# Kernel tuning notes

Measured on AMD Instinct MI355X. Metric: run time of the kernel, lower is better.

The kernel has to match this reference:

```python
import jax, jax.numpy as jnp
import numpy as np

B, S, H, E = 64, 1024, 256, 256

def setup_inputs() -> dict:
    key = jax.random.key(0)
    k = jax.random.split(key, 6)
    scale = 1.0 / np.sqrt(H)
    return {
        "data_alpha": jax.random.normal(k[0], (B, S, H), jnp.float32),
        "data_beta": jax.random.normal(k[1], (B, S, H), jnp.float32),
        "data_embed": jax.random.normal(k[2], (B, S, E), jnp.float32),
        "data_mask": jnp.ones((B, S), jnp.float32),
        "Wb": jax.random.normal(k[3], (E, H), jnp.float32) * scale,
        "bb": jnp.zeros((E,), jnp.float32),
        "Wa": jax.random.normal(k[4], (H,), jnp.float32) * scale,
        "ba": jnp.zeros((1,), jnp.float32),
    }

def reference(data_alpha, data_beta, data_embed, data_mask, Wb, bb, Wa, ba):
    # beta gates: tanh(Linear(H->E))  [B,S,E]
    beta_w = jnp.tanh(jnp.einsum('bsh,eh->bse', data_beta, Wb) + bb)
    # alpha logits: Linear(H->1)  [B,S]
    corr = jnp.einsum('bsh,h->bs', data_alpha, Wa) + ba
    attn = jnp.exp(corr)[:, None, :]                       # [B,1,S]
    seq = data_alpha.shape[1]
    flag = jnp.triu(jnp.ones((seq, seq), data_alpha.dtype))[None]  # j >= i
    ef = flag * data_mask[:, None, :]                      # [B,S,S]
    num = attn * ef                                        # [B,S,S]
    acc = jnp.sum(num, axis=-1, keepdims=True) + 1e-10     # [B,S,1]
    alpha = num / acc                                      # [B,S,S]
    ew = beta_w * data_embed                               # [B,S,E]
    return jnp.einsum('bij,bje->bie', alpha, ew)           # [B,S,E]
```

## Files before the change

### kernel.cpp

```cpp
#include <hip/hip_runtime.h>
#include <hip/hip_bf16.h>

#define B_ 64
#define S_ 1024
#define H_ 256
#define E_ 256
#define C_ 16
#define CS_ 64

#define LDSB_STRIDE 40

typedef __attribute__((ext_vector_type(8))) __bf16 bf16x8;
typedef __attribute__((ext_vector_type(4))) __bf16 bf16x4;
typedef __attribute__((ext_vector_type(4))) float f32x4;

__global__ __launch_bounds__(256, 4) void k2_fused(
        const float* __restrict__ alpha, const float* __restrict__ beta,
        const float* __restrict__ embed, const float* __restrict__ mask,
        const float* __restrict__ Wb,    const float* __restrict__ bb,
        const float* __restrict__ Wa,    const float* __restrict__ ba,
        float* __restrict__ w, float* __restrict__ chunkTot, float* __restrict__ t) {
    __shared__ __bf16 ldsB[E_ * LDSB_STRIDE];
    __shared__ float red[4 * E_];
    __shared__ float wsh[CS_];

    const int tid = threadIdx.x;
    const int wv = tid >> 6, lane = tid & 63;
    const int l15 = lane & 15, q = lane >> 4;
    const int m0 = blockIdx.x * CS_;

    const float4 waf = *(const float4*)(Wa + lane * 4);
    const float ba0 = ba[0];
    for (int i = 0; i < 16; ++i) {
        int m = m0 + wv * 16 + i;
        float4 a = *(const float4*)(alpha + (size_t)m * H_ + lane * 4);
        float p = a.x * waf.x + a.y * waf.y + a.z * waf.z + a.w * waf.w;
        #pragma unroll
        for (int off = 32; off > 0; off >>= 1) p += __shfl_xor(p, off, 64);
        if (lane == 0) {
            float wm = __expf(p + ba0) * mask[m];
            wsh[wv * 16 + i] = wm;
            w[m] = wm;
        }
    }

    const float* Arow = beta + (size_t)(m0 + wv * 16 + l15) * H_;
    f32x4 acc[16];
    #pragma unroll
    for (int i = 0; i < 16; ++i) acc[i] = (f32x4){0.f, 0.f, 0.f, 0.f};

    const int ebase = tid >> 3;
    const int kj = (tid & 7) * 4;

    for (int kc = 0; kc < 8; ++kc) {
        int koff = kc * 32 + q * 8;
        float4 a0 = *(const float4*)(Arow + koff);
        float4 a1 = *(const float4*)(Arow + koff + 4);

        #pragma unroll
        for (int pass = 0; pass < 8; ++pass) {
            int e = pass * 32 + ebase;
            float4 v = *(const float4*)(Wb + (size_t)e * H_ + kc * 32 + kj);
            bf16x4 bv;
            bv[0] = (__bf16)v.x; bv[1] = (__bf16)v.y;
            bv[2] = (__bf16)v.z; bv[3] = (__bf16)v.w;
            *(bf16x4*)(ldsB + e * LDSB_STRIDE + kj) = bv;
        }
        __syncthreads();

        bf16x8 af;
        af[0] = (__bf16)a0.x; af[1] = (__bf16)a0.y;
        af[2] = (__bf16)a0.z; af[3] = (__bf16)a0.w;
        af[4] = (__bf16)a1.x; af[5] = (__bf16)a1.y;
        af[6] = (__bf16)a1.z; af[7] = (__bf16)a1.w;
        #pragma unroll
        for (int et = 0; et < 16; ++et) {
            bf16x8 bf = *(const bf16x8*)(ldsB + (et * 16 + l15) * LDSB_STRIDE + q * 8);
            acc[et] = __builtin_amdgcn_mfma_f32_16x16x32_bf16(af, bf, acc[et], 0, 0, 0);
        }
        __syncthreads();
    }

    float colsum[16];
    #pragma unroll
    for (int et = 0; et < 16; ++et) {
        int e = et * 16 + l15;
        float bbe = bb[e];
        float cs = 0.f;
        #pragma unroll
        for (int r = 0; r < 4; ++r) {
            int m = m0 + wv * 16 + q * 4 + r;
            float x = acc[et][r] + bbe;
            x = fminf(fmaxf(x, -15.f), 15.f);
            float ex = __expf(2.f * x);
            float th = (ex - 1.f) / (ex + 1.f);
            float tv = wsh[wv * 16 + q * 4 + r] * th * embed[(size_t)m * E_ + e];
            t[(size_t)m * E_ + e] = tv;
            cs += tv;
        }
        colsum[et] = cs;
    }
    #pragma unroll
    for (int et = 0; et < 16; ++et) {
        float c = colsum[et];
        c += __shfl_xor(c, 16, 64);
        c += __shfl_xor(c, 32, 64);
        if (q == 0) red[wv * E_ + et * 16 + l15] = c;
    }
    __syncthreads();
    float ct = red[0 * E_ + tid] + red[1 * E_ + tid] + red[2 * E_ + tid] + red[3 * E_ + tid];
    chunkTot[(size_t)blockIdx.x * E_ + tid] = ct;
}

__global__ __launch_bounds__(256) void k3b_scan(
        const float* __restrict__ w, const float* __restrict__ chunkTot,
        float* __restrict__ chunkOff, float* __restrict__ invDen) {
    const int tid = threadIdx.x;
    const int b = blockIdx.x;

    float acc = 0.f;
    #pragma unroll
    for (int c = C_ - 1; c >= 0; --c) {
        chunkOff[((size_t)b * C_ + c) * E_ + tid] = acc;
        acc += chunkTot[((size_t)b * C_ + c) * E_ + tid];
    }

    float4 w4 = *(const float4*)(w + b * S_ + tid * 4);
    float tot = w4.x + w4.y + w4.z + w4.w;
    int lane = tid & 63, wv = tid >> 6;
    float suf = tot;
    #pragma unroll
    for (int off = 1; off < 64; off <<= 1) {
        float o = __shfl_down(suf, off, 64);
        if (lane + off < 64) suf += o;
    }
    __shared__ float wsum[4];
    if (lane == 0) wsum[wv] = suf;
    __syncthreads();
    float waveOff = 0.f;
    for (int j = wv + 1; j < 4; ++j) waveOff += wsum[j];
    float after = (suf - tot) + waveOff;
    float s3 = w4.w + after;
    float s2 = w4.z + s3;
    float s1 = w4.y + s2;
    float s0 = w4.x + s1;
    float4 inv = { 1.f / (s0 + 1e-10f), 1.f / (s1 + 1e-10f),
                   1.f / (s2 + 1e-10f), 1.f / (s3 + 1e-10f) };
    *(float4*)(invDen + b * S_ + tid * 4) = inv;
}

__global__ __launch_bounds__(256) void k3c_finish(
        float* __restrict__ t, const float* __restrict__ chunkOff,
        const float* __restrict__ invDen) {
    const int b = blockIdx.x >> 4, c = blockIdx.x & 15;
    const int e = threadIdx.x;
    float acc = chunkOff[(size_t)blockIdx.x * E_ + e];
    const float* iv = invDen + b * S_ + c * CS_;
    float* tp = t + ((size_t)b * S_ + c * CS_) * E_ + e;
    #pragma unroll 4
    for (int s = CS_ - 1; s >= 0; --s) {
        float v = tp[(size_t)s * E_];
        acc += v;
        tp[(size_t)s * E_] = acc * iv[s];
    }
}

extern "C" void kernel_launch(void* const* d_in, const int* in_sizes, int n_in,
                              void* d_out, int out_size, void* d_ws, size_t ws_size,
                              hipStream_t stream) {
    const float* alpha = (const float*)d_in[0];
    const float* beta  = (const float*)d_in[1];
    const float* embed = (const float*)d_in[2];
    const float* mask  = (const float*)d_in[3];
    const float* Wb    = (const float*)d_in[4];
    const float* bb    = (const float*)d_in[5];
    const float* Wa    = (const float*)d_in[6];
    const float* ba    = (const float*)d_in[7];

    float* t = (float*)d_out;

    char* ws = (char*)d_ws;
    float* w        = (float*)ws;
    float* chunkTot = (float*)(ws + (256 << 10));
    float* chunkOff = (float*)(ws + (256 << 10) + (1 << 20));
    float* invDen   = (float*)(ws + (256 << 10) + (2 << 20));

    k2_fused<<<B_ * C_, 256, 0, stream>>>(alpha, beta, embed, mask, Wb, bb, Wa, ba,
                                          w, chunkTot, t);
    k3b_scan<<<B_, 256, 0, stream>>>(w, chunkTot, chunkOff, invDen);
    k3c_finish<<<B_ * C_, 256, 0, stream>>>(t, chunkOff, invDen);
}
```

Measured before the change: 280.5 us.

## Pre-convert Wb to bf16, do in-chunk suffix scan in fused kernel, vectorize finish

A new tiny kernel converts Wb to bf16 once per call, so the fused kernel loads MFMA B operands straight from global/L2 instead of converting and staging them through LDS with two barriers per k-step. The fused kernel now does the within-chunk suffix scan itself, using register partials, cross-quad shuffles and per-wave totals in LDS, so the finish kernel becomes a fully parallel float4 add-offset-and-scale pass instead of a serial 64-step column scan. The alpha logit dot product is also restructured to four threads per row. The cost is an extra launch and uncoalesced-ish per-lane B loads from global memory instead of LDS.

```diff
diff --git a/kernel.cpp b/kernel.cpp
--- a/kernel.cpp
+++ b/kernel.cpp
@@ -8,19 +8,26 @@
 #define C_ 16
 #define CS_ 64
 
-#define LDSB_STRIDE 40
-
 typedef __attribute__((ext_vector_type(8))) __bf16 bf16x8;
 typedef __attribute__((ext_vector_type(4))) __bf16 bf16x4;
 typedef __attribute__((ext_vector_type(4))) float f32x4;
 
+__global__ __launch_bounds__(256) void k0_wb_bf16(const float* __restrict__ Wb,
+                                                  __bf16* __restrict__ WbBf) {
+    int i = blockIdx.x * 256 + threadIdx.x;
+    float4 v = ((const float4*)Wb)[i];
+    bf16x4 b;
+    b[0] = (__bf16)v.x; b[1] = (__bf16)v.y;
+    b[2] = (__bf16)v.z; b[3] = (__bf16)v.w;
+    ((bf16x4*)WbBf)[i] = b;
+}
+
 __global__ __launch_bounds__(256, 4) void k2_fused(
         const float* __restrict__ alpha, const float* __restrict__ beta,
         const float* __restrict__ embed, const float* __restrict__ mask,
-        const float* __restrict__ Wb,    const float* __restrict__ bb,
+        const __bf16* __restrict__ WbBf, const float* __restrict__ bb,
         const float* __restrict__ Wa,    const float* __restrict__ ba,
         float* __restrict__ w, float* __restrict__ chunkTot, float* __restrict__ t) {
-    __shared__ __bf16 ldsB[E_ * LDSB_STRIDE];
     __shared__ float red[4 * E_];
     __shared__ float wsh[CS_];
 
@@ -29,45 +36,37 @@
     const int l15 = lane & 15, q = lane >> 4;
     const int m0 = blockIdx.x * CS_;
 
-    const float4 waf = *(const float4*)(Wa + lane * 4);
-    const float ba0 = ba[0];
-    for (int i = 0; i < 16; ++i) {
-        int m = m0 + wv * 16 + i;
-        float4 a = *(const float4*)(alpha + (size_t)m * H_ + lane * 4);
-        float p = a.x * waf.x + a.y * waf.y + a.z * waf.z + a.w * waf.w;
-        #pragma unroll
-        for (int off = 32; off > 0; off >>= 1) p += __shfl_xor(p, off, 64);
-        if (lane == 0) {
-            float wm = __expf(p + ba0) * mask[m];
-            wsh[wv * 16 + i] = wm;
+    {
+        const int pr = tid >> 2, pc = tid & 3;
+        const int m = m0 + pr;
+        const float4* ar = (const float4*)(alpha + (size_t)m * H_ + pc * 64);
+        const float4* wr = (const float4*)(Wa + pc * 64);
+        float p = 0.f;
+        #pragma unroll
+        for (int i = 0; i < 16; ++i) {
+            float4 a = ar[i], v = wr[i];
+            p += a.x * v.x + a.y * v.y + a.z * v.z + a.w * v.w;
+        }
+        p += __shfl_xor(p, 1, 64);
+        p += __shfl_xor(p, 2, 64);
+        if (pc == 0) {
+            float wm = __expf(p + ba[0]) * mask[m];
+            wsh[pr] = wm;
             w[m] = wm;
         }
     }
-
-    const float* Arow = beta + (size_t)(m0 + wv * 16 + l15) * H_;
+    __syncthreads();
+
+    const float*  Arow = beta + (size_t)(m0 + wv * 16 + l15) * H_ + q * 8;
+    const __bf16* Brow = WbBf + (size_t)l15 * H_ + q * 8;
     f32x4 acc[16];
     #pragma unroll
     for (int i = 0; i < 16; ++i) acc[i] = (f32x4){0.f, 0.f, 0.f, 0.f};
 
-    const int ebase = tid >> 3;
-    const int kj = (tid & 7) * 4;
-
+    #pragma unroll 2
     for (int kc = 0; kc < 8; ++kc) {
-        int koff = kc * 32 + q * 8;
-        float4 a0 = *(const float4*)(Arow + koff);
-        float4 a1 = *(const float4*)(Arow + koff + 4);
-
-        #pragma unroll
-        for (int pass = 0; pass < 8; ++pass) {
-            int e = pass * 32 + ebase;
-            float4 v = *(const float4*)(Wb + (size_t)e * H_ + kc * 32 + kj);
-            bf16x4 bv;
-            bv[0] = (__bf16)v.x; bv[1] = (__bf16)v.y;
-            bv[2] = (__bf16)v.z; bv[3] = (__bf16)v.w;
-            *(bf16x4*)(ldsB + e * LDSB_STRIDE + kj) = bv;
-        }
-        __syncthreads();
-
+        float4 a0 = *(const float4*)(Arow + kc * 32);
+        float4 a1 = *(const float4*)(Arow + kc * 32 + 4);
         bf16x8 af;
         af[0] = (__bf16)a0.x; af[1] = (__bf16)a0.y;
         af[2] = (__bf16)a0.z; af[3] = (__bf16)a0.w;
@@ -75,40 +74,60 @@
         af[6] = (__bf16)a1.z; af[7] = (__bf16)a1.w;
         #pragma unroll
         for (int et = 0; et < 16; ++et) {
-            bf16x8 bf = *(const bf16x8*)(ldsB + (et * 16 + l15) * LDSB_STRIDE + q * 8);
+            bf16x8 bf = *(const bf16x8*)(Brow + (size_t)et * 16 * H_ + kc * 32);
             acc[et] = __builtin_amdgcn_mfma_f32_16x16x32_bf16(af, bf, acc[et], 0, 0, 0);
         }
-        __syncthreads();
-    }
-
-    float colsum[16];
+    }
+
+    float wmr[4];
+    #pragma unroll
+    for (int r = 0; r < 4; ++r) wmr[r] = wsh[wv * 16 + q * 4 + r];
+
     #pragma unroll
     for (int et = 0; et < 16; ++et) {
-        int e = et * 16 + l15;
-        float bbe = bb[e];
-        float cs = 0.f;
+        const int e = et * 16 + l15;
+        const float bbe = bb[e];
+        float tv[4];
         #pragma unroll
         for (int r = 0; r < 4; ++r) {
-            int m = m0 + wv * 16 + q * 4 + r;
+            const int m = m0 + wv * 16 + q * 4 + r;
             float x = acc[et][r] + bbe;
             x = fminf(fmaxf(x, -15.f), 15.f);
             float ex = __expf(2.f * x);
             float th = (ex - 1.f) / (ex + 1.f);
-            float tv = wsh[wv * 16 + q * 4 + r] * th * embed[(size_t)m * E_ + e];
-            t[(size_t)m * E_ + e] = tv;
-            cs += tv;
-        }
-        colsum[et] = cs;
-    }
+            tv[r] = wmr[r] * th * embed[(size_t)m * E_ + e];
+        }
+        float s3 = tv[3];
+        float s2 = tv[2] + s3;
+        float s1 = tv[1] + s2;
+        float s0 = tv[0] + s1;
+        float g  = s0;
+        float g1 = __shfl_down(g, 16, 64);
+        float g2 = __shfl_down(g, 32, 64);
+        float g3 = __shfl_down(g, 48, 64);
+        float addG = (q < 3 ? g1 : 0.f) + (q < 2 ? g2 : 0.f) + (q < 1 ? g3 : 0.f);
+        if (q == 0) red[wv * E_ + e] = g + addG;
+        acc[et][0] = s0 + addG;
+        acc[et][1] = s1 + addG;
+        acc[et][2] = s2 + addG;
+        acc[et][3] = s3 + addG;
+    }
+    __syncthreads();
+
     #pragma unroll
     for (int et = 0; et < 16; ++et) {
-        float c = colsum[et];
-        c += __shfl_xor(c, 16, 64);
-        c += __shfl_xor(c, 32, 64);
-        if (q == 0) red[wv * E_ + et * 16 + l15] = c;
-    }
-    __syncthreads();
-    float ct = red[0 * E_ + tid] + red[1 * E_ + tid] + red[2 * E_ + tid] + red[3 * E_ + tid];
+        const int e = et * 16 + l15;
+        float wa = 0.f;
+        #pragma unroll
+        for (int d = 1; d < 4; ++d)
+            if (wv + d < 4) wa += red[(wv + d) * E_ + e];
+        #pragma unroll
+        for (int r = 0; r < 4; ++r) {
+            const int m = m0 + wv * 16 + q * 4 + r;
+            t[(size_t)m * E_ + e] = acc[et][r] + wa;
+        }
+    }
+    const float ct = red[tid] + red[E_ + tid] + red[2 * E_ + tid] + red[3 * E_ + tid];
     chunkTot[(size_t)blockIdx.x * E_ + tid] = ct;
 }
 
@@ -152,16 +171,25 @@
 __global__ __launch_bounds__(256) void k3c_finish(
         float* __restrict__ t, const float* __restrict__ chunkOff,
         const float* __restrict__ invDen) {
-    const int b = blockIdx.x >> 4, c = blockIdx.x & 15;
-    const int e = threadIdx.x;
-    float acc = chunkOff[(size_t)blockIdx.x * E_ + e];
+    const int blk = blockIdx.x;
+    const int b = blk >> 4, c = blk & 15;
+    const int tid = threadIdx.x;
+    float4* tp = (float4*)(t + ((size_t)b * S_ + c * CS_) * E_);
+    const float4* co = (const float4*)(chunkOff + (size_t)blk * E_);
     const float* iv = invDen + b * S_ + c * CS_;
-    float* tp = t + ((size_t)b * S_ + c * CS_) * E_ + e;
-    #pragma unroll 4
-    for (int s = CS_ - 1; s >= 0; --s) {
-        float v = tp[(size_t)s * E_];
-        acc += v;
-        tp[(size_t)s * E_] = acc * iv[s];
+    #pragma unroll
+    for (int i = 0; i < 16; ++i) {
+        const int idx = i * 256 + tid;
+        const int row = idx >> 6;
+        const int e4 = idx & 63;
+        float4 v = tp[idx];
+        float4 o = co[e4];
+        float s = iv[row];
+        v.x = (v.x + o.x) * s;
+        v.y = (v.y + o.y) * s;
+        v.z = (v.z + o.z) * s;
+        v.w = (v.w + o.w) * s;
+        tp[idx] = v;
     }
 }
 
@@ -180,12 +208,14 @@
     float* t = (float*)d_out;
 
     char* ws = (char*)d_ws;
-    float* w        = (float*)ws;
-    float* chunkTot = (float*)(ws + (256 << 10));
-    float* chunkOff = (float*)(ws + (256 << 10) + (1 << 20));
-    float* invDen   = (float*)(ws + (256 << 10) + (2 << 20));
-
-    k2_fused<<<B_ * C_, 256, 0, stream>>>(alpha, beta, embed, mask, Wb, bb, Wa, ba,
+    float*  w        = (float*)ws;
+    float*  chunkTot = (float*)(ws + (256 << 10));
+    float*  chunkOff = (float*)(ws + (256 << 10) + (1 << 20));
+    float*  invDen   = (float*)(ws + (256 << 10) + (2 << 20));
+    __bf16* WbBf     = (__bf16*)(ws + (512 << 10) + (2 << 20));
+
+    k0_wb_bf16<<<E_ * H_ / 1024, 256, 0, stream>>>(Wb, WbBf);
+    k2_fused<<<B_ * C_, 256, 0, stream>>>(alpha, beta, embed, mask, WbBf, bb, Wa, ba,
                                           w, chunkTot, t);
     k3b_scan<<<B_, 256, 0, stream>>>(w, chunkTot, chunkOff, invDen);
     k3c_finish<<<B_ * C_, 256, 0, stream>>>(t, chunkOff, invDen);
```

Result: slower. 303.0 us (+8.0%).
